# Optimization experiments

Hardware: AMD Instinct MI355X
Metric: run time of the kernel (lower is better)

The kernel has to match this reference:

```python
import jax, jax.numpy as jnp
import numpy as np

# Static config (matches init_kwargs)
B, S, D = 1, 2048, 2048
H, KVH, HD = 16, 4, 128
GROUPS = H // KVH
HEAVY_RATIO = 0.1
RECENT_RATIO = 0.1
SCALE = HD ** -0.5


def setup_inputs() -> dict:
    key = jax.random.key(0)
    ks = jax.random.split(key, 8)
    std = 0.02
    return {
        "hidden_states": jax.random.normal(ks[0], (B, S, D), jnp.float32),
        "q_w": jax.random.normal(ks[1], (D, H * HD), jnp.float32) * std,
        "q_b": jax.random.normal(ks[2], (H * HD,), jnp.float32) * std,
        "k_w": jax.random.normal(ks[3], (D, KVH * HD), jnp.float32) * std,
        "k_b": jax.random.normal(ks[4], (KVH * HD,), jnp.float32) * std,
        "v_w": jax.random.normal(ks[5], (D, KVH * HD), jnp.float32) * std,
        "v_b": jax.random.normal(ks[6], (KVH * HD,), jnp.float32) * std,
        "o_w": jax.random.normal(ks[7], (H * HD, D), jnp.float32) * std,
    }


def reference(hidden_states, q_w, q_b, k_w, k_b, v_w, v_b, o_w):
    # QKV projections -> [B, heads, S, HD]
    q = (hidden_states @ q_w + q_b).reshape(B, S, H, HD).transpose(0, 2, 1, 3)
    k = (hidden_states @ k_w + k_b).reshape(B, S, KVH, HD).transpose(0, 2, 1, 3)
    v = (hidden_states @ v_w + v_b).reshape(B, S, KVH, HD).transpose(0, 2, 1, 3)

    # GQA: repeat KV heads to match query heads (repeat_kv)
    k = jnp.repeat(k, GROUPS, axis=1)  # [B, H, S, HD]
    v = jnp.repeat(v, GROUPS, axis=1)

    # Scaled QK^T with additive causal mask (first call: no H2O mask yet)
    scores = jnp.einsum("bhqd,bhkd->bhqk", q, k) * SCALE
    causal = jnp.tril(jnp.ones((S, S), dtype=bool))
    scores = jnp.where(causal[None, None], scores, jnp.finfo(scores.dtype).min)

    # Softmax in fp32, cast back
    probs = jax.nn.softmax(scores.astype(jnp.float32), axis=-1).astype(q.dtype)

    # H2O heavy-hitter scoring: accumulate attn mass per key, per head
    cur_scores = probs.sum(axis=0).sum(axis=1)  # [H, S]

    heavy_budget = int(HEAVY_RATIO * S)
    recent_budget = int(RECENT_RATIO * S)

    # Eviction mask for next step: keep recent window + top-k heavy hitters
    attn_mask = jnp.ones((H, S + 1), dtype=probs.dtype)
    attn_mask = attn_mask.at[:, : S + 1 - recent_budget].set(0.0)
    selected = cur_scores[:, : S - recent_budget]  # scores outside recent window
    _, keep_topk = jax.lax.top_k(selected, heavy_budget)  # [H, heavy_budget]
    attn_mask = attn_mask.at[jnp.arange(H)[:, None], keep_topk].set(1.0)

    # Attention output + output projection
    out = jnp.einsum("bhqk,bhkd->bhqd", probs, v)
    out = out.transpose(0, 2, 1, 3).reshape(B, S, H * HD) @ o_w
    return out, attn_mask
```

## Files before the change

### kernel.cpp

```cpp
#include <hip/hip_runtime.h>
#include <hip/hip_bf16.h>
#include <math.h>

constexpr int S   = 2048;
constexpr int D   = 2048;
constexpr int H   = 16;
constexpr int KVH = 4;
constexpr int HD  = 128;
constexpr int NQ  = H * HD;
constexpr int NKV = KVH * HD;
constexpr int N3  = NQ + 2 * NKV;
constexpr int GROUPS = H / KVH;
constexpr float SCALE = 0.088388347648318447f;
constexpr int HEAVY  = 204;
constexpr int RECENT = 204;
constexpr int SKEEP  = S - RECENT;
constexpr int MASKC  = S + 1;
constexpr int NTILE_H = 528;

typedef short bf16x8 __attribute__((ext_vector_type(8)));
typedef _Float16 f16x8 __attribute__((ext_vector_type(8)));
typedef unsigned short ushort8 __attribute__((ext_vector_type(8)));
typedef unsigned short ushort4v __attribute__((ext_vector_type(4)));
typedef float f32x4 __attribute__((ext_vector_type(4)));

__device__ __forceinline__ unsigned short f2b(float x) {
  __hip_bfloat16 h = __float2bfloat16(x);
  return *(unsigned short*)&h;
}
__device__ __forceinline__ float b2f(unsigned short u) {
  __hip_bfloat16 h = *(__hip_bfloat16*)&u;
  return __bfloat162float(h);
}
__device__ __forceinline__ unsigned short f2h(float x) {
  _Float16 h = (_Float16)x;
  return *(unsigned short*)&h;
}

__device__ __forceinline__ void gload16(const unsigned short* g,
                                        unsigned short* l) {
  __builtin_amdgcn_global_load_lds(
      (const __attribute__((address_space(1))) unsigned int*)g,
      (__attribute__((address_space(3))) unsigned int*)l, 16, 0, 0);
}

__device__ __forceinline__ void split_wT_dev(
    const float* __restrict__ in, unsigned short* __restrict__ oh,
    unsigned short* __restrict__ ol, int K, int N, int rowOff, int ldOut,
    int bx, int by, float (*Lt)[65]) {
  const int n0 = bx * 64, k0 = by * 64;
  const int t = threadIdx.x;
  const int cq = t & 15, r4 = t >> 4;
#pragma unroll
  for (int i = 0; i < 4; ++i) {
    int r = r4 + i * 16;
    float4 v = *(const float4*)&in[(size_t)(k0 + r) * N + n0 + cq * 4];
    Lt[cq * 4 + 0][r] = v.x;
    Lt[cq * 4 + 1][r] = v.y;
    Lt[cq * 4 + 2][r] = v.z;
    Lt[cq * 4 + 3][r] = v.w;
  }
  __syncthreads();
#pragma unroll
  for (int i = 0; i < 4; ++i) {
    int rr = r4 + i * 16;
    size_t base = (size_t)(rowOff + n0 + rr) * ldOut + k0 + cq * 4;
    ushort4v hv, lv;
#pragma unroll
    for (int j = 0; j < 4; ++j) {
      float x = Lt[rr][cq * 4 + j];
      unsigned short h = f2b(x);
      hv[j] = h;
      lv[j] = f2b(x - b2f(h));
    }
    *(ushort4v*)&oh[base] = hv;
    *(ushort4v*)&ol[base] = lv;
  }
}

__global__ __launch_bounds__(256) void prep_all(
    const float* __restrict__ hs, const float* __restrict__ q_w,
    const float* __restrict__ k_w, const float* __restrict__ v_w,
    const float* __restrict__ o_w, const float* __restrict__ qb,
    const float* __restrict__ kb, const float* __restrict__ vb,
    unsigned short* __restrict__ hsh, unsigned short* __restrict__ hsl,
    unsigned short* __restrict__ WTh, unsigned short* __restrict__ WTl,
    unsigned short* __restrict__ OTh, float* __restrict__ bcat) {
  __shared__ float Lt[64][65];
  const int b = blockIdx.x;
  if (b < 1024) {
    split_wT_dev(q_w, WTh, WTl, D, NQ, 0, D, b & 31, b >> 5, Lt);
  } else if (b < 1280) {
    int b2 = b - 1024;
    split_wT_dev(k_w, WTh, WTl, D, NKV, NQ, D, b2 & 7, b2 >> 3, Lt);
  } else if (b < 1536) {
    int b2 = b - 1280;
    split_wT_dev(v_w, WTh, WTl, D, NKV, NQ + NKV, D, b2 & 7, b2 >> 3, Lt);
  } else if (b < 2560) {
    int b2 = b - 1536;
    const int n0 = (b2 & 31) * 64, k0 = (b2 >> 5) * 64;
    const int t = threadIdx.x;
    const int cq = t & 15, r4 = t >> 4;
#pragma unroll
    for (int i = 0; i < 4; ++i) {
      int r = r4 + i * 16;
      float4 v = *(const float4*)&o_w[(size_t)(k0 + r) * D + n0 + cq * 4];
      Lt[cq * 4 + 0][r] = v.x;
      Lt[cq * 4 + 1][r] = v.y;
      Lt[cq * 4 + 2][r] = v.z;
      Lt[cq * 4 + 3][r] = v.w;
    }
    __syncthreads();
#pragma unroll
    for (int i = 0; i < 4; ++i) {
      int rr = r4 + i * 16;
      size_t base = (size_t)(n0 + rr) * NQ + k0 + cq * 4;
      ushort4v hv;
#pragma unroll
      for (int j = 0; j < 4; ++j) hv[j] = f2b(Lt[rr][cq * 4 + j]);
      *(ushort4v*)&OTh[base] = hv;
    }
  } else if (b < 3072) {
    int b2 = b - 2560;
    size_t base = (size_t)b2 * 8192;
    for (int i = threadIdx.x * 4; i < 8192; i += 1024) {
      float4 v = *(const float4*)&hs[base + i];
      ushort4v hv, lv;
      float xs[4] = {v.x, v.y, v.z, v.w};
#pragma unroll
      for (int j = 0; j < 4; ++j) {
        unsigned short h = f2b(xs[j]);
        hv[j] = h;
        lv[j] = f2b(xs[j] - b2f(h));
      }
      *(ushort4v*)&hsh[base + i] = hv;
      *(ushort4v*)&hsl[base + i] = lv;
    }
  } else {
    int i = (b - 3072) * 256 + threadIdx.x;
    if (i < NQ) bcat[i] = qb[i];
    else if (i < NQ + NKV) bcat[i] = kb[i - NQ];
    else if (i < N3) bcat[i] = vb[i - NQ - NKV];
  }
}

__global__ __launch_bounds__(256) void gemm_qkv(
    const unsigned short* __restrict__ Ah, const unsigned short* __restrict__ Al,
    const unsigned short* __restrict__ Bh, const unsigned short* __restrict__ Bl,
    const float* __restrict__ bias,
    unsigned short* __restrict__ Qh,
    unsigned short* __restrict__ Kh,
    unsigned short* __restrict__ Vt, int M, int N, int K) {
  __shared__ __align__(16) unsigned short sAh[2][128 * 32];
  __shared__ __align__(16) unsigned short sAl[2][128 * 32];
  __shared__ __align__(16) unsigned short sBh[2][96 * 32];
  __shared__ __align__(16) unsigned short sBl[2][96 * 32];
  const int tid = threadIdx.x;
  const int lane = tid & 63, wave = tid >> 6;
  const int wm = wave >> 1, wn = wave & 1;
  const int quad = lane >> 4, l16 = lane & 15;
  const int m0 = blockIdx.y * 128, n0 = blockIdx.x * 96;

  const int lr = lane >> 2;
  const int gj = (lane & 3) ^ (lr & 3);

  f32x4 acc[4][3];
#pragma unroll
  for (int i = 0; i < 4; ++i)
#pragma unroll
    for (int j = 0; j < 3; ++j) acc[i][j] = (f32x4){0.f, 0.f, 0.f, 0.f};

#pragma unroll
  for (int it = 0; it < 2; ++it) {
    int c = wave * 2 + it;
    int r = c * 16 + lr;
    size_t ga = (size_t)(m0 + r) * K + gj * 8;
    gload16(&Ah[ga], &sAh[0][c * 512]);
    gload16(&Al[ga], &sAl[0][c * 512]);
  }
#pragma unroll
  for (int it = 0; it < 2; ++it) {
    int c = wave + it * 4;
    if (c < 6) {
      int r = c * 16 + lr;
      size_t gb = (size_t)(n0 + r) * K + gj * 8;
      gload16(&Bh[gb], &sBh[0][c * 512]);
      gload16(&Bl[gb], &sBl[0][c * 512]);
    }
  }
  __syncthreads();

  int cur = 0;
  for (int k0 = 0; k0 < K; k0 += 32, cur ^= 1) {
    if (k0 + 32 < K) {
      const int kn = k0 + 32;
#pragma unroll
      for (int it = 0; it < 2; ++it) {
        int c = wave * 2 + it;
        int r = c * 16 + lr;
        size_t ga = (size_t)(m0 + r) * K + kn + gj * 8;
        gload16(&Ah[ga], &sAh[cur ^ 1][c * 512]);
        gload16(&Al[ga], &sAl[cur ^ 1][c * 512]);
      }
#pragma unroll
      for (int it = 0; it < 2; ++it) {
        int c = wave + it * 4;
        if (c < 6) {
          int r = c * 16 + lr;
          size_t gb = (size_t)(n0 + r) * K + kn + gj * 8;
          gload16(&Bh[gb], &sBh[cur ^ 1][c * 512]);
          gload16(&Bl[gb], &sBl[cur ^ 1][c * 512]);
        }
      }
    }
    const int sw = (quad ^ (l16 & 3)) * 8;
    bf16x8 fah[4], fal[4], fbh[3], fbl[3];
#pragma unroll
    for (int i = 0; i < 4; ++i) {
      int ra = (wm * 64 + i * 16 + l16) * 32 + sw;
      fah[i] = *(bf16x8*)&sAh[cur][ra];
      fal[i] = *(bf16x8*)&sAl[cur][ra];
    }
#pragma unroll
    for (int j = 0; j < 3; ++j) {
      int rb = (wn * 48 + j * 16 + l16) * 32 + sw;
      fbh[j] = *(bf16x8*)&sBh[cur][rb];
      fbl[j] = *(bf16x8*)&sBl[cur][rb];
    }
#pragma unroll
    for (int i = 0; i < 4; ++i)
#pragma unroll
      for (int j = 0; j < 3; ++j) {
        acc[i][j] = __builtin_amdgcn_mfma_f32_16x16x32_bf16(fah[i], fbh[j], acc[i][j], 0, 0, 0);
        acc[i][j] = __builtin_amdgcn_mfma_f32_16x16x32_bf16(fah[i], fbl[j], acc[i][j], 0, 0, 0);
        acc[i][j] = __builtin_amdgcn_mfma_f32_16x16x32_bf16(fal[i], fbh[j], acc[i][j], 0, 0, 0);
      }
    __syncthreads();
  }
#pragma unroll
  for (int i = 0; i < 4; ++i) {
#pragma unroll
    for (int j = 0; j < 3; ++j) {
      int row = m0 + wm * 64 + i * 16 + quad * 4;
      int col = n0 + wn * 48 + j * 16 + l16;
      float bv = bias[col];
      if (col < NQ) {
#pragma unroll
        for (int r = 0; r < 4; ++r) {
          size_t o = (size_t)(row + r) * NQ + col;
          Qh[o] = f2h(acc[i][j][r] + bv);
        }
      } else if (col < NQ + NKV) {
        int c = col - NQ;
        size_t ob = ((size_t)(c >> 7) * S) * HD + (c & 127);
#pragma unroll
        for (int r = 0; r < 4; ++r) {
          size_t o = ob + (size_t)(row + r) * HD;
          Kh[o] = f2h(acc[i][j][r] + bv);
        }
      } else {
        int c = col - NQ - NKV;
        ushort4v pv;
#pragma unroll
        for (int r = 0; r < 4; ++r) pv[r] = f2h(acc[i][j][r] + bv);
        *(ushort4v*)&Vt[((size_t)(c >> 7) * HD + (c & 127)) * S + row] = pv;
      }
    }
  }
}

__global__ __launch_bounds__(256) void fuse_post(
    const unsigned short* __restrict__ AOh, const unsigned short* __restrict__ OTh,
    float* __restrict__ C,
    const unsigned short* __restrict__ Eg, const float* __restrict__ lbuf,
    float* __restrict__ cur) {
  __shared__ __align__(16) unsigned char smem[32768];
  const int bid = blockIdx.x;
  const int tid = threadIdx.x;
  if (bid < 256) {
    unsigned short* sAb = (unsigned short*)smem;
    unsigned short* sBb = (unsigned short*)smem + 8192;
    const int lane = tid & 63, wave = tid >> 6;
    const int wm = wave >> 1, wn = wave & 1;
    const int quad = lane >> 4, l16 = lane & 15;
    const int m0 = (bid >> 4) * 128, n0 = (bid & 15) * 128;
    const int K = NQ, N = D;
    const int lr = lane >> 2;
    const int gj = (lane & 3) ^ (lr & 3);

    f32x4 acc[4][4];
#pragma unroll
    for (int i = 0; i < 4; ++i)
#pragma unroll
      for (int j = 0; j < 4; ++j) acc[i][j] = (f32x4){0.f, 0.f, 0.f, 0.f};

#pragma unroll
    for (int it = 0; it < 2; ++it) {
      int c = wave * 2 + it;
      int r = c * 16 + lr;
      size_t ga = (size_t)(m0 + r) * K + gj * 8;
      size_t gb = (size_t)(n0 + r) * K + gj * 8;
      gload16(&AOh[ga], &sAb[c * 512]);
      gload16(&OTh[gb], &sBb[c * 512]);
    }
    __syncthreads();

    int cb = 0;
    for (int k0 = 0; k0 < K; k0 += 32, cb ^= 1) {
      if (k0 + 32 < K) {
        const int kn = k0 + 32;
#pragma unroll
        for (int it = 0; it < 2; ++it) {
          int c = wave * 2 + it;
          int r = c * 16 + lr;
          size_t ga = (size_t)(m0 + r) * K + kn + gj * 8;
          size_t gb = (size_t)(n0 + r) * K + kn + gj * 8;
          gload16(&AOh[ga], &sAb[(cb ^ 1) * 4096 + c * 512]);
          gload16(&OTh[gb], &sBb[(cb ^ 1) * 4096 + c * 512]);
        }
      }
      const int sw = (quad ^ (l16 & 3)) * 8;
      bf16x8 fa[4], fb[4];
#pragma unroll
      for (int i = 0; i < 4; ++i) {
        fa[i] = *(bf16x8*)&sAb[cb * 4096 + (wm * 64 + i * 16 + l16) * 32 + sw];
        fb[i] = *(bf16x8*)&sBb[cb * 4096 + (wn * 64 + i * 16 + l16) * 32 + sw];
      }
#pragma unroll
      for (int i = 0; i < 4; ++i)
#pragma unroll
        for (int j = 0; j < 4; ++j)
          acc[i][j] = __builtin_amdgcn_mfma_f32_16x16x32_bf16(fa[i], fb[j], acc[i][j], 0, 0, 0);
      __syncthreads();
    }
#pragma unroll
    for (int i = 0; i < 4; ++i)
#pragma unroll
      for (int j = 0; j < 4; ++j) {
        int row = m0 + wm * 64 + i * 16 + quad * 4;
        int col = n0 + wn * 64 + j * 16 + l16;
#pragma unroll
        for (int r = 0; r < 4; ++r)
          C[(size_t)(row + r) * N + col] = acc[i][j][r];
      }
  } else {
    const int bid2 = bid - 256;
    const int kt = bid2 % 29;
    const int h  = bid2 / 29;
    const int c8 = tid & 7, qg = tid >> 3;
    float acc[8];
#pragma unroll
    for (int j = 0; j < 8; ++j) acc[j] = 0.f;
    const size_t hb = (size_t)h * NTILE_H;
    for (int qt = kt; qt < 32; ++qt) {
      size_t tb = (hb + (size_t)(qt * (qt + 1) / 2) + kt) * 4096;
      float li0 = 1.0f / lbuf[h * S + qt * 64 + qg];
      float li1 = 1.0f / lbuf[h * S + qt * 64 + 32 + qg];
      f16x8 e0 = *(const f16x8*)&Eg[tb + (size_t)qg * 64 + c8 * 8];
      f16x8 e1 = *(const f16x8*)&Eg[tb + (size_t)(32 + qg) * 64 + c8 * 8];
#pragma unroll
      for (int j = 0; j < 8; ++j)
        acc[j] += (float)e0[j] * li0 + (float)e1[j] * li1;
    }
    float (*red)[8] = (float(*)[8])smem;
#pragma unroll
    for (int j = 0; j < 8; ++j) red[tid][j] = acc[j];
    __syncthreads();
    if (tid < 64) {
      int cc = tid >> 3, j = tid & 7;
      float s = 0.f;
#pragma unroll
      for (int g = 0; g < 32; ++g) s += red[cc + 8 * g][j];
      cur[h * S + kt * 64 + cc * 8 + j] = s;
    }
  }
}

__global__ __launch_bounds__(256) void gemm_bf16(
    const unsigned short* __restrict__ Ah, const unsigned short* __restrict__ Bh,
    float* __restrict__ C, int M, int N, int K) {
  __shared__ __align__(16) unsigned short sA[2][128 * 32];
  __shared__ __align__(16) unsigned short sB[2][128 * 32];
  const int tid = threadIdx.x;
  const int lane = tid & 63, wave = tid >> 6;
  const int wm = wave >> 1, wn = wave & 1;
  const int quad = lane >> 4, l16 = lane & 15;
  const int m0 = blockIdx.y * 128, n0 = blockIdx.x * 128;
  const int lr = lane >> 2;
  const int gj = (lane & 3) ^ (lr & 3);

  f32x4 acc[4][4];
#pragma unroll
  for (int i = 0; i < 4; ++i)
#pragma unroll
    for (int j = 0; j < 4; ++j) acc[i][j] = (f32x4){0.f, 0.f, 0.f, 0.f};

#pragma unroll
  for (int it = 0; it < 2; ++it) {
    int c = wave * 2 + it;
    int r = c * 16 + lr;
    size_t ga = (size_t)(m0 + r) * K + gj * 8;
    size_t gb = (size_t)(n0 + r) * K + gj * 8;
    gload16(&Ah[ga], &sA[0][c * 512]);
    gload16(&Bh[gb], &sB[0][c * 512]);
  }
  __syncthreads();

  int cur = 0;
  for (int k0 = 0; k0 < K; k0 += 32, cur ^= 1) {
    if (k0 + 32 < K) {
      const int kn = k0 + 32;
#pragma unroll
      for (int it = 0; it < 2; ++it) {
        int c = wave * 2 + it;
        int r = c * 16 + lr;
        size_t ga = (size_t)(m0 + r) * K + kn + gj * 8;
        size_t gb = (size_t)(n0 + r) * K + kn + gj * 8;
        gload16(&Ah[ga], &sA[cur ^ 1][c * 512]);
        gload16(&Bh[gb], &sB[cur ^ 1][c * 512]);
      }
    }
    const int sw = (quad ^ (l16 & 3)) * 8;
    bf16x8 fa[4], fb[4];
#pragma unroll
    for (int i = 0; i < 4; ++i) {
      fa[i] = *(bf16x8*)&sA[cur][(wm * 64 + i * 16 + l16) * 32 + sw];
      fb[i] = *(bf16x8*)&sB[cur][(wn * 64 + i * 16 + l16) * 32 + sw];
    }
#pragma unroll
    for (int i = 0; i < 4; ++i)
#pragma unroll
      for (int j = 0; j < 4; ++j)
        acc[i][j] = __builtin_amdgcn_mfma_f32_16x16x32_bf16(fa[i], fb[j], acc[i][j], 0, 0, 0);
    __syncthreads();
  }
#pragma unroll
  for (int i = 0; i < 4; ++i)
#pragma unroll
    for (int j = 0; j < 4; ++j) {
      int row = m0 + wm * 64 + i * 16 + quad * 4;
      int col = n0 + wn * 64 + j * 16 + l16;
#pragma unroll
      for (int r = 0; r < 4; ++r)
        C[(size_t)(row + r) * N + col] = acc[i][j][r];
    }
}

__global__ __launch_bounds__(256) void attn_mfma(
    const unsigned short* __restrict__ Qh,
    const unsigned short* __restrict__ Kh,
    const unsigned short* __restrict__ Vt, unsigned short* __restrict__ AOh,
    float* __restrict__ lbuf, unsigned short* __restrict__ Eg) {
  const int x = blockIdx.x;
  const int base = x & 255;
  const int qt0 = base & 31, h0 = base >> 5;
  const int qt = (x < 256) ? qt0 : 31 - qt0;
  const int h  = (x < 256) ? h0 : h0 + 8;
  const int kvh = h / GROUPS;
  const int tid = threadIdx.x;
  const int lane = tid & 63, w = tid >> 6;
  const int quad = lane >> 4, l16 = lane & 15;
  const int q0 = qt * 64;

  __shared__ __align__(16) unsigned short smem[22528];
  unsigned short* sQ  = smem;
  unsigned short* sK  = smem;
  unsigned short* sVt = smem + 8704;
  unsigned short* sP  = smem + 17920;

  const size_t ebase = ((size_t)h * NTILE_H + (size_t)(qt * (qt + 1) / 2)) * 4096;

  ushort8 pK[4], pV[4];
#pragma unroll
  for (int it = 0; it < 4; ++it) {
    int idx = tid + it * 256;
    int r = idx >> 4, c8 = idx & 15;
    size_t g = ((size_t)kvh * S + r) * HD + c8 * 8;
    pK[it] = *(const ushort8*)&Kh[g];
  }
#pragma unroll
  for (int it = 0; it < 4; ++it) {
    int idx = tid + it * 256;
    int d = idx >> 3, c8 = idx & 7;
    size_t g = ((size_t)kvh * HD + d) * S + c8 * 8;
    pV[it] = *(const ushort8*)&Vt[g];
  }

#pragma unroll
  for (int it = 0; it < 4; ++it) {
    int idx = tid + it * 256;
    int r = idx >> 4, c8 = idx & 15;
    size_t g = (size_t)(q0 + r) * NQ + h * HD + c8 * 8;
    *(ushort8*)&sQ[r * 136 + c8 * 8] = *(const ushort8*)&Qh[g];
  }
  __syncthreads();
  f16x8 fq[4];
#pragma unroll
  for (int d4 = 0; d4 < 4; ++d4)
    fq[d4] = *(f16x8*)&sQ[(w * 16 + l16) * 136 + d4 * 32 + quad * 8];

  f32x4 O[8];
#pragma unroll
  for (int jn = 0; jn < 8; ++jn) O[jn] = (f32x4){0.f, 0.f, 0.f, 0.f};
  float l_[4] = {0.f, 0.f, 0.f, 0.f};

  const int row_l = w * 16 + quad * 4;
  const int wbase = w * 1152;

  for (int kt = 0; kt <= qt; ++kt) {
    __syncthreads();
#pragma unroll
    for (int it = 0; it < 4; ++it) {
      int idx = tid + it * 256;
      int r = idx >> 4, c8 = idx & 15;
      *(ushort8*)&sK[r * 136 + c8 * 8] = pK[it];
    }
#pragma unroll
    for (int it = 0; it < 4; ++it) {
      int idx = tid + it * 256;
      int d = idx >> 3, c8 = idx & 7;
      *(ushort8*)&sVt[d * 72 + c8 * 8] = pV[it];
    }
    __syncthreads();
    if (kt < qt) {
#pragma unroll
      for (int it = 0; it < 4; ++it) {
        int idx = tid + it * 256;
        int r = idx >> 4, c8 = idx & 15;
        size_t g = ((size_t)kvh * S + (kt + 1) * 64 + r) * HD + c8 * 8;
        pK[it] = *(const ushort8*)&Kh[g];
      }
#pragma unroll
      for (int it = 0; it < 4; ++it) {
        int idx = tid + it * 256;
        int d = idx >> 3, c8 = idx & 7;
        size_t g = ((size_t)kvh * HD + d) * S + (kt + 1) * 64 + c8 * 8;
        pV[it] = *(const ushort8*)&Vt[g];
      }
    }

    f32x4 sc[4];
#pragma unroll
    for (int j = 0; j < 4; ++j) sc[j] = (f32x4){0.f, 0.f, 0.f, 0.f};
#pragma unroll
    for (int d4 = 0; d4 < 4; ++d4) {
#pragma unroll
      for (int j = 0; j < 4; ++j) {
        f16x8 bk = *(f16x8*)&sK[(j * 16 + l16) * 136 + d4 * 32 + quad * 8];
        sc[j] = __builtin_amdgcn_mfma_f32_16x16x32_f16(fq[d4], bk, sc[j], 0, 0, 0);
      }
    }
    const bool diag = (kt == qt);
#pragma unroll
    for (int j = 0; j < 4; ++j) {
      int col_l = j * 16 + l16;
#pragma unroll
      for (int r = 0; r < 4; ++r) {
        float v = sc[j][r] * SCALE;
        if (diag && col_l > row_l + r) v = -INFINITY;
        float p = __expf(v);
        sc[j][r] = p;
        l_[r] += p;
      }
    }
#pragma unroll
    for (int j = 0; j < 4; ++j)
#pragma unroll
      for (int r = 0; r < 4; ++r)
        sP[wbase + (quad * 4 + r) * 72 + j * 16 + l16] = f2h(sc[j][r]);

    if (Eg) {
      size_t tb = ebase + (size_t)kt * 4096;
#pragma unroll
      for (int it2 = 0; it2 < 2; ++it2) {
        int ci = lane + it2 * 64;
        int row = ci >> 3, cc = ci & 7;
        *(ushort8*)&Eg[tb + (size_t)(w * 16 + row) * 64 + cc * 8] =
            *(ushort8*)&sP[wbase + row * 72 + cc * 8];
      }
    }

    f16x8 ap0 = *(f16x8*)&sP[wbase + l16 * 72 + quad * 8];
    f16x8 ap1 = *(f16x8*)&sP[wbase + l16 * 72 + 32 + quad * 8];
#pragma unroll
    for (int jn = 0; jn < 8; ++jn) {
      f16x8 bv0 = *(f16x8*)&sVt[(jn * 16 + l16) * 72 + quad * 8];
      f16x8 bv1 = *(f16x8*)&sVt[(jn * 16 + l16) * 72 + 32 + quad * 8];
      O[jn] = __builtin_amdgcn_mfma_f32_16x16x32_f16(ap0, bv0, O[jn], 0, 0, 0);
      O[jn] = __builtin_amdgcn_mfma_f32_16x16x32_f16(ap1, bv1, O[jn], 0, 0, 0);
    }
  }
#pragma unroll
  for (int off = 1; off < 16; off <<= 1)
#pragma unroll
    for (int r = 0; r < 4; ++r) l_[r] += __shfl_xor(l_[r], off);
  float linv[4];
#pragma unroll
  for (int r = 0; r < 4; ++r) linv[r] = 1.0f / l_[r];
#pragma unroll
  for (int jn = 0; jn < 8; ++jn)
#pragma unroll
    for (int r = 0; r < 4; ++r)
      AOh[(size_t)(q0 + row_l + r) * NQ + h * HD + jn * 16 + l16] =
          f2b(O[jn][r] * linv[r]);
  if (l16 == 0) {
#pragma unroll
    for (int r = 0; r < 4; ++r)
      lbuf[h * S + q0 + row_l + r] = l_[r];
  }
}

__global__ __launch_bounds__(256) void cur_mfma(
    const unsigned short* __restrict__ Qh,
    const unsigned short* __restrict__ Kh,
    const float* __restrict__ lbuf, float* __restrict__ cur) {
  const int x = blockIdx.x;
  const int base = x & 255;
  const int kt0 = base & 31, h0 = base >> 5;
  const int kt = (x < 256) ? kt0 : 31 - kt0;
  const int h  = (x < 256) ? h0 : h0 + 8;
  const int kvh = h / GROUPS;
  const int tid = threadIdx.x;
  const int lane = tid & 63, w = tid >> 6;
  const int quad = lane >> 4, l16 = lane & 15;

  __shared__ __align__(16) unsigned short sKh[8704];
  __shared__ __align__(16) unsigned short sQh[8704];
  __shared__ float slinv[64];

#pragma unroll
  for (int it = 0; it < 4; ++it) {
    int idx = tid + it * 256;
    int r = idx >> 4, c8 = idx & 15;
    size_t g = ((size_t)kvh * S + kt * 64 + r) * HD + c8 * 8;
    *(ushort8*)&sKh[r * 136 + c8 * 8] = *(const ushort8*)&Kh[g];
  }
  __syncthreads();
  f16x8 fk[4];
#pragma unroll
  for (int d4 = 0; d4 < 4; ++d4)
    fk[d4] = *(f16x8*)&sKh[(w * 16 + l16) * 136 + d4 * 32 + quad * 8];

  const int krow_l = w * 16 + quad * 4;
  float csum[4] = {0.f, 0.f, 0.f, 0.f};

  ushort8 pQ[4];
  float pli = 0.f;
#pragma unroll
  for (int it = 0; it < 4; ++it) {
    int idx = tid + it * 256;
    int r = idx >> 4, c8 = idx & 15;
    size_t g = (size_t)(kt * 64 + r) * NQ + h * HD + c8 * 8;
    pQ[it] = *(const ushort8*)&Qh[g];
  }
  if (tid < 64) pli = 1.0f / lbuf[h * S + kt * 64 + tid];

  for (int qt = kt; qt < S / 64; ++qt) {
    __syncthreads();
#pragma unroll
    for (int it = 0; it < 4; ++it) {
      int idx = tid + it * 256;
      int r = idx >> 4, c8 = idx & 15;
      *(ushort8*)&sQh[r * 136 + c8 * 8] = pQ[it];
    }
    if (tid < 64) slinv[tid] = pli;
    __syncthreads();
    if (qt + 1 < S / 64) {
#pragma unroll
      for (int it = 0; it < 4; ++it) {
        int idx = tid + it * 256;
        int r = idx >> 4, c8 = idx & 15;
        size_t g = (size_t)((qt + 1) * 64 + r) * NQ + h * HD + c8 * 8;
        pQ[it] = *(const ushort8*)&Qh[g];
      }
      if (tid < 64) pli = 1.0f / lbuf[h * S + (qt + 1) * 64 + tid];
    }
    f32x4 sc[4];
#pragma unroll
    for (int j = 0; j < 4; ++j) sc[j] = (f32x4){0.f, 0.f, 0.f, 0.f};
#pragma unroll
    for (int d4 = 0; d4 < 4; ++d4) {
#pragma unroll
      for (int j = 0; j < 4; ++j) {
        f16x8 bq = *(f16x8*)&sQh[(j * 16 + l16) * 136 + d4 * 32 + quad * 8];
        sc[j] = __builtin_amdgcn_mfma_f32_16x16x32_f16(fk[d4], bq, sc[j], 0, 0, 0);
      }
    }
    const bool diag = (qt == kt);
#pragma unroll
    for (int j = 0; j < 4; ++j) {
      int qcol_l = j * 16 + l16;
      float lv = slinv[qcol_l];
#pragma unroll
      for (int r = 0; r < 4; ++r) {
        float p = __expf(sc[j][r] * SCALE) * lv;
        if (diag && (krow_l + r) > qcol_l) p = 0.f;
        csum[r] += p;
      }
    }
  }
#pragma unroll
  for (int off = 1; off < 16; off <<= 1)
#pragma unroll
    for (int r = 0; r < 4; ++r) csum[r] += __shfl_xor(csum[r], off);
  if (l16 == 0) {
#pragma unroll
    for (int r = 0; r < 4; ++r)
      cur[h * S + kt * 64 + krow_l + r] = csum[r];
  }
}

__global__ __launch_bounds__(256) void topk_kernel(
    const float* __restrict__ cur, float* __restrict__ mask) {
  const int h = blockIdx.x;
  const int tid = threadIdx.x;
  const int lane = tid & 63, w = tid >> 6;
  __shared__ unsigned uv[SKEEP];
  __shared__ int redw[4];
  __shared__ int wsum[4];

  for (int i = tid; i < SKEEP; i += 256) uv[i] = __float_as_uint(cur[h * S + i]);
  __syncthreads();

  unsigned lo = 0u, hi = 0xffffffffu;
  while (lo < hi) {
    unsigned mid = (unsigned)((((unsigned long long)lo + hi) + 1ull) >> 1);
    int c = 0;
    for (int i = tid; i < SKEEP; i += 256) c += (uv[i] >= mid) ? 1 : 0;
#pragma unroll
    for (int off = 1; off < 64; off <<= 1) c += __shfl_xor(c, off);
    if (lane == 0) redw[w] = c;
    __syncthreads();
    int cnt = redw[0] + redw[1] + redw[2] + redw[3];
    __syncthreads();
    if (cnt >= HEAVY) lo = mid; else hi = mid - 1;
  }
  const unsigned vk = lo;
  int c = 0;
  for (int i = tid; i < SKEEP; i += 256) c += (uv[i] > vk) ? 1 : 0;
#pragma unroll
  for (int off = 1; off < 64; off <<= 1) c += __shfl_xor(c, off);
  if (lane == 0) redw[w] = c;
  __syncthreads();
  const int cgt = redw[0] + redw[1] + redw[2] + redw[3];
  const int rem = HEAVY - cgt;

  for (int j = tid; j < MASKC; j += 256)
    mask[(size_t)h * MASKC + j] = (j >= MASKC - RECENT) ? 1.0f : 0.0f;
  __syncthreads();
  for (int i = tid; i < SKEEP; i += 256)
    if (uv[i] > vk) mask[(size_t)h * MASKC + i] = 1.0f;

  constexpr int PER = (SKEEP + 255) / 256;
  int i0 = tid * PER;
  int i1 = i0 + PER;
  if (i0 > SKEEP) i0 = SKEEP;
  if (i1 > SKEEP) i1 = SKEEP;
  int myT = 0;
  for (int i = i0; i < i1; ++i) myT += (uv[i] == vk) ? 1 : 0;
  int v = myT;
#pragma unroll
  for (int off = 1; off < 64; off <<= 1) {
    int t = __shfl_up(v, off);
    if (lane >= off) v += t;
  }
  if (lane == 63) wsum[w] = v;
  __syncthreads();
  int wOff = 0;
  for (int k = 0; k < w; ++k) wOff += wsum[k];
  int excl = wOff + v - myT;
  for (int i = i0; i < i1; ++i) {
    if (uv[i] == vk) {
      if (excl < rem) mask[(size_t)h * MASKC + i] = 1.0f;
      ++excl;
    }
  }
}

extern "C" void kernel_launch(void* const* d_in, const int* in_sizes, int n_in,
                              void* d_out, int out_size, void* d_ws,
                              size_t ws_size, hipStream_t stream) {
  const float* hs  = (const float*)d_in[0];
  const float* q_w = (const float*)d_in[1];
  const float* q_b = (const float*)d_in[2];
  const float* k_w = (const float*)d_in[3];
  const float* k_b = (const float*)d_in[4];
  const float* v_w = (const float*)d_in[5];
  const float* v_b = (const float*)d_in[6];
  const float* o_w = (const float*)d_in[7];

  char* ws = (char*)d_ws;
  unsigned short* Qh   = (unsigned short*)(ws + 0);
  unsigned short* Kh   = (unsigned short*)(ws + 16777216);
  unsigned short* Vt   = (unsigned short*)(ws + 20971520);
  unsigned short* AOh  = (unsigned short*)(ws + 25165824);
  float* lb   = (float*)(ws + 33685504);
  float* cur  = (float*)(ws + 33816576);
  float* bcat = (float*)(ws + 33947648);
  char* pool = ws + 33959936;
  unsigned short* hsh = (unsigned short*)pool;
  unsigned short* hsl = (unsigned short*)(pool + 8388608);
  unsigned short* WTh = (unsigned short*)(pool + 16777216);
  unsigned short* WTl = (unsigned short*)(pool + 29360128);
  unsigned short* OTh = (unsigned short*)(pool + 41943040);

  const size_t E_OFF = 84291584ull;
  const size_t E_SZ  = (size_t)H * NTILE_H * 4096 * 2;
  const bool use_e = (ws_size >= E_OFF + E_SZ);
  unsigned short* Eg = use_e ? (unsigned short*)(ws + E_OFF) : nullptr;

  float* outp  = (float*)d_out;
  float* maskp = outp + (size_t)S * D;

  dim3 blk(256);
  prep_all<<<dim3(3084), blk, 0, stream>>>(hs, q_w, k_w, v_w, o_w, q_b, k_b,
                                           v_b, hsh, hsl, WTh, WTl, OTh, bcat);
  gemm_qkv<<<dim3(N3 / 96, S / 128), blk, 0, stream>>>(
      hsh, hsl, WTh, WTl, bcat, Qh, Kh, Vt, S, N3, D);
  attn_mfma<<<dim3(512), blk, 0, stream>>>(Qh, Kh, Vt, AOh, lb, Eg);
  if (use_e) {
    fuse_post<<<dim3(256 + 29 * 16), blk, 0, stream>>>(AOh, OTh, outp, Eg, lb,
                                                       cur);
    topk_kernel<<<dim3(H), blk, 0, stream>>>(cur, maskp);
  } else {
    cur_mfma<<<dim3(512), blk, 0, stream>>>(Qh, Kh, lb, cur);
    topk_kernel<<<dim3(H), blk, 0, stream>>>(cur, maskp);
    gemm_bf16<<<dim3(D / 128, S / 128), blk, 0, stream>>>(AOh, OTh, outp, S, D,
                                                          NQ);
  }
}
```

Baseline: 289.5 us.

## Move o_w transpose into attention launch and halve output GEMM tile width

The o_w transpose/bf16 conversion moves out of prep_all and into 1024 extra blocks of the attn_mfma launch, where it can fill idle CUs alongside the causal-attention blocks. The output-projection part of fuse_post now uses 128x64 tiles (512 blocks instead of 256), giving more parallelism and a smaller shared-memory footprint. The tradeoff is more redundant A-tile loads across tiles. If use_e is false, the fallback gemm_bf16 still reads OTh, which is now produced by attn_mfma, so launch order still holds.

```diff
diff --git a/kernel.cpp b/kernel.cpp
--- a/kernel.cpp
+++ b/kernel.cpp
@@ -81,11 +81,11 @@
 __global__ __launch_bounds__(256) void prep_all(
     const float* __restrict__ hs, const float* __restrict__ q_w,
     const float* __restrict__ k_w, const float* __restrict__ v_w,
-    const float* __restrict__ o_w, const float* __restrict__ qb,
-    const float* __restrict__ kb, const float* __restrict__ vb,
+    const float* __restrict__ qb, const float* __restrict__ kb,
+    const float* __restrict__ vb,
     unsigned short* __restrict__ hsh, unsigned short* __restrict__ hsl,
     unsigned short* __restrict__ WTh, unsigned short* __restrict__ WTl,
-    unsigned short* __restrict__ OTh, float* __restrict__ bcat) {
+    float* __restrict__ bcat) {
   __shared__ float Lt[64][65];
   const int b = blockIdx.x;
   if (b < 1024) {
@@ -96,32 +96,8 @@
   } else if (b < 1536) {
     int b2 = b - 1280;
     split_wT_dev(v_w, WTh, WTl, D, NKV, NQ + NKV, D, b2 & 7, b2 >> 3, Lt);
-  } else if (b < 2560) {
+  } else if (b < 2048) {
     int b2 = b - 1536;
-    const int n0 = (b2 & 31) * 64, k0 = (b2 >> 5) * 64;
-    const int t = threadIdx.x;
-    const int cq = t & 15, r4 = t >> 4;
-#pragma unroll
-    for (int i = 0; i < 4; ++i) {
-      int r = r4 + i * 16;
-      float4 v = *(const float4*)&o_w[(size_t)(k0 + r) * D + n0 + cq * 4];
-      Lt[cq * 4 + 0][r] = v.x;
-      Lt[cq * 4 + 1][r] = v.y;
-      Lt[cq * 4 + 2][r] = v.z;
-      Lt[cq * 4 + 3][r] = v.w;
-    }
-    __syncthreads();
-#pragma unroll
-    for (int i = 0; i < 4; ++i) {
-      int rr = r4 + i * 16;
-      size_t base = (size_t)(n0 + rr) * NQ + k0 + cq * 4;
-      ushort4v hv;
-#pragma unroll
-      for (int j = 0; j < 4; ++j) hv[j] = f2b(Lt[rr][cq * 4 + j]);
-      *(ushort4v*)&OTh[base] = hv;
-    }
-  } else if (b < 3072) {
-    int b2 = b - 2560;
     size_t base = (size_t)b2 * 8192;
     for (int i = threadIdx.x * 4; i < 8192; i += 1024) {
       float4 v = *(const float4*)&hs[base + i];
@@ -137,7 +113,7 @@
       *(ushort4v*)&hsl[base + i] = lv;
     }
   } else {
-    int i = (b - 3072) * 256 + threadIdx.x;
+    int i = (b - 2048) * 256 + threadIdx.x;
     if (i < NQ) bcat[i] = qb[i];
     else if (i < NQ + NKV) bcat[i] = kb[i - NQ];
     else if (i < N3) bcat[i] = vb[i - NQ - NKV];
@@ -274,34 +250,37 @@
     float* __restrict__ C,
     const unsigned short* __restrict__ Eg, const float* __restrict__ lbuf,
     float* __restrict__ cur) {
-  __shared__ __align__(16) unsigned char smem[32768];
+  __shared__ __align__(16) unsigned char smem[24576];
   const int bid = blockIdx.x;
   const int tid = threadIdx.x;
-  if (bid < 256) {
+  if (bid < 512) {
     unsigned short* sAb = (unsigned short*)smem;
     unsigned short* sBb = (unsigned short*)smem + 8192;
     const int lane = tid & 63, wave = tid >> 6;
     const int wm = wave >> 1, wn = wave & 1;
     const int quad = lane >> 4, l16 = lane & 15;
-    const int m0 = (bid >> 4) * 128, n0 = (bid & 15) * 128;
+    const int m0 = (bid >> 5) * 128, n0 = (bid & 31) * 64;
     const int K = NQ, N = D;
     const int lr = lane >> 2;
     const int gj = (lane & 3) ^ (lr & 3);
 
-    f32x4 acc[4][4];
+    f32x4 acc[4][2];
 #pragma unroll
     for (int i = 0; i < 4; ++i)
 #pragma unroll
-      for (int j = 0; j < 4; ++j) acc[i][j] = (f32x4){0.f, 0.f, 0.f, 0.f};
+      for (int j = 0; j < 2; ++j) acc[i][j] = (f32x4){0.f, 0.f, 0.f, 0.f};
 
 #pragma unroll
     for (int it = 0; it < 2; ++it) {
       int c = wave * 2 + it;
       int r = c * 16 + lr;
       size_t ga = (size_t)(m0 + r) * K + gj * 8;
+      gload16(&AOh[ga], &sAb[c * 512]);
+    }
+    {
+      int r = wave * 16 + lr;
       size_t gb = (size_t)(n0 + r) * K + gj * 8;
-      gload16(&AOh[ga], &sAb[c * 512]);
-      gload16(&OTh[gb], &sBb[c * 512]);
+      gload16(&OTh[gb], &sBb[wave * 512]);
     }
     __syncthreads();
 
@@ -314,37 +293,41 @@
           int c = wave * 2 + it;
           int r = c * 16 + lr;
           size_t ga = (size_t)(m0 + r) * K + kn + gj * 8;
+          gload16(&AOh[ga], &sAb[(cb ^ 1) * 4096 + c * 512]);
+        }
+        {
+          int r = wave * 16 + lr;
           size_t gb = (size_t)(n0 + r) * K + kn + gj * 8;
-          gload16(&AOh[ga], &sAb[(cb ^ 1) * 4096 + c * 512]);
-          gload16(&OTh[gb], &sBb[(cb ^ 1) * 4096 + c * 512]);
+          gload16(&OTh[gb], &sBb[(cb ^ 1) * 2048 + wave * 512]);
         }
       }
       const int sw = (quad ^ (l16 & 3)) * 8;
-      bf16x8 fa[4], fb[4];
-#pragma unroll
-      for (int i = 0; i < 4; ++i) {
+      bf16x8 fa[4], fb[2];
+#pragma unroll
+      for (int i = 0; i < 4; ++i)
         fa[i] = *(bf16x8*)&sAb[cb * 4096 + (wm * 64 + i * 16 + l16) * 32 + sw];
-        fb[i] = *(bf16x8*)&sBb[cb * 4096 + (wn * 64 + i * 16 + l16) * 32 + sw];
-      }
+#pragma unroll
+      for (int j = 0; j < 2; ++j)
+        fb[j] = *(bf16x8*)&sBb[cb * 2048 + (wn * 32 + j * 16 + l16) * 32 + sw];
 #pragma unroll
       for (int i = 0; i < 4; ++i)
 #pragma unroll
-        for (int j = 0; j < 4; ++j)
+        for (int j = 0; j < 2; ++j)
           acc[i][j] = __builtin_amdgcn_mfma_f32_16x16x32_bf16(fa[i], fb[j], acc[i][j], 0, 0, 0);
       __syncthreads();
     }
 #pragma unroll
     for (int i = 0; i < 4; ++i)
 #pragma unroll
-      for (int j = 0; j < 4; ++j) {
+      for (int j = 0; j < 2; ++j) {
         int row = m0 + wm * 64 + i * 16 + quad * 4;
-        int col = n0 + wn * 64 + j * 16 + l16;
+        int col = n0 + wn * 32 + j * 16 + l16;
 #pragma unroll
         for (int r = 0; r < 4; ++r)
           C[(size_t)(row + r) * N + col] = acc[i][j][r];
       }
   } else {
-    const int bid2 = bid - 256;
+    const int bid2 = bid - 512;
     const int kt = bid2 % 29;
     const int h  = bid2 / 29;
     const int c8 = tid & 7, qg = tid >> 3;
@@ -450,19 +433,49 @@
     const unsigned short* __restrict__ Qh,
     const unsigned short* __restrict__ Kh,
     const unsigned short* __restrict__ Vt, unsigned short* __restrict__ AOh,
-    float* __restrict__ lbuf, unsigned short* __restrict__ Eg) {
+    float* __restrict__ lbuf, unsigned short* __restrict__ Eg,
+    const float* __restrict__ o_w, unsigned short* __restrict__ OTh) {
   const int x = blockIdx.x;
+  const int tid = threadIdx.x;
+
+  __shared__ __align__(16) unsigned short smem[22528];
+
+  if (x >= 512) {
+    float (*Lt)[65] = (float(*)[65])smem;
+    int b2 = x - 512;
+    const int n0 = (b2 & 31) * 64, k0 = (b2 >> 5) * 64;
+    const int cq = tid & 15, r4 = tid >> 4;
+#pragma unroll
+    for (int i = 0; i < 4; ++i) {
+      int r = r4 + i * 16;
+      float4 v = *(const float4*)&o_w[(size_t)(k0 + r) * D + n0 + cq * 4];
+      Lt[cq * 4 + 0][r] = v.x;
+      Lt[cq * 4 + 1][r] = v.y;
+      Lt[cq * 4 + 2][r] = v.z;
+      Lt[cq * 4 + 3][r] = v.w;
+    }
+    __syncthreads();
+#pragma unroll
+    for (int i = 0; i < 4; ++i) {
+      int rr = r4 + i * 16;
+      size_t base = (size_t)(n0 + rr) * NQ + k0 + cq * 4;
+      ushort4v hv;
+#pragma unroll
+      for (int j = 0; j < 4; ++j) hv[j] = f2b(Lt[rr][cq * 4 + j]);
+      *(ushort4v*)&OTh[base] = hv;
+    }
+    return;
+  }
+
   const int base = x & 255;
   const int qt0 = base & 31, h0 = base >> 5;
   const int qt = (x < 256) ? qt0 : 31 - qt0;
   const int h  = (x < 256) ? h0 : h0 + 8;
   const int kvh = h / GROUPS;
-  const int tid = threadIdx.x;
   const int lane = tid & 63, w = tid >> 6;
   const int quad = lane >> 4, l16 = lane & 15;
   const int q0 = qt * 64;
 
-  __shared__ __align__(16) unsigned short smem[22528];
   unsigned short* sQ  = smem;
   unsigned short* sK  = smem;
   unsigned short* sVt = smem + 8704;
@@ -813,13 +826,13 @@
   float* maskp = outp + (size_t)S * D;
 
   dim3 blk(256);
-  prep_all<<<dim3(3084), blk, 0, stream>>>(hs, q_w, k_w, v_w, o_w, q_b, k_b,
-                                           v_b, hsh, hsl, WTh, WTl, OTh, bcat);
+  prep_all<<<dim3(2060), blk, 0, stream>>>(hs, q_w, k_w, v_w, q_b, k_b, v_b,
+                                           hsh, hsl, WTh, WTl, bcat);
   gemm_qkv<<<dim3(N3 / 96, S / 128), blk, 0, stream>>>(
       hsh, hsl, WTh, WTl, bcat, Qh, Kh, Vt, S, N3, D);
-  attn_mfma<<<dim3(512), blk, 0, stream>>>(Qh, Kh, Vt, AOh, lb, Eg);
+  attn_mfma<<<dim3(1536), blk, 0, stream>>>(Qh, Kh, Vt, AOh, lb, Eg, o_w, OTh);
   if (use_e) {
-    fuse_post<<<dim3(256 + 29 * 16), blk, 0, stream>>>(AOh, OTh, outp, Eg, lb,
+    fuse_post<<<dim3(512 + 29 * 16), blk, 0, stream>>>(AOh, OTh, outp, Eg, lb,
                                                        cur);
     topk_kernel<<<dim3(H), blk, 0, stream>>>(cur, maskp);
   } else {
```

New measurement: 293.5 us. No clear change (+1.4%).

## Split KV range for long query tiles in attention and add combine kernel

Applied to the files above, without the earlier changes.

For query tiles in the upper half of the causal triangle, the attention kernel now splits the key range into two halves handled by separate blocks. Each block writes unnormalized fp32 partial outputs and row sums, and a new combine kernel adds them, normalizes, and writes the bf16 output and row sums. The aim is to shorten the critical path of the longest causal tiles and improve load balance, raising the grid from 512 to 768 blocks. The cost is an extra kernel launch and fp32 partial-result traffic, and the path only runs when the workspace is large enough.

```diff
diff --git a/kernel.cpp b/kernel.cpp
--- a/kernel.cpp
+++ b/kernel.cpp
@@ -450,17 +450,43 @@
     const unsigned short* __restrict__ Qh,
     const unsigned short* __restrict__ Kh,
     const unsigned short* __restrict__ Vt, unsigned short* __restrict__ AOh,
-    float* __restrict__ lbuf, unsigned short* __restrict__ Eg) {
+    float* __restrict__ lbuf, unsigned short* __restrict__ Eg,
+    int do_split, float* __restrict__ Opart, float* __restrict__ lpart) {
   const int x = blockIdx.x;
-  const int base = x & 255;
-  const int qt0 = base & 31, h0 = base >> 5;
-  const int qt = (x < 256) ? qt0 : 31 - qt0;
-  const int h  = (x < 256) ? h0 : h0 + 8;
-  const int kvh = h / GROUPS;
   const int tid = threadIdx.x;
   const int lane = tid & 63, w = tid >> 6;
   const int quad = lane >> 4, l16 = lane & 15;
+
+  int qt, h, kt0, kt1, part = 0;
+  bool partial = false;
+  if (do_split) {
+    if (x < 512) {
+      qt = 31 - (x >> 5);
+      int r5 = x & 31;
+      h = r5 >> 1;
+      part = r5 & 1;
+      int nh = (qt + 1) >> 1;
+      kt0 = part ? nh : 0;
+      kt1 = part ? qt + 1 : nh;
+      partial = true;
+    } else {
+      int s2 = x - 512;
+      qt = 15 - (s2 >> 4);
+      h = s2 & 15;
+      kt0 = 0;
+      kt1 = qt + 1;
+    }
+  } else {
+    const int base = x & 255;
+    const int qt0v = base & 31, h0 = base >> 5;
+    qt = (x < 256) ? qt0v : 31 - qt0v;
+    h  = (x < 256) ? h0 : h0 + 8;
+    kt0 = 0;
+    kt1 = qt + 1;
+  }
+  const int kvh = h / GROUPS;
   const int q0 = qt * 64;
+  const int pairIdx = partial ? ((qt - 16) * 16 + h) : 0;
 
   __shared__ __align__(16) unsigned short smem[22528];
   unsigned short* sQ  = smem;
@@ -475,14 +501,14 @@
   for (int it = 0; it < 4; ++it) {
     int idx = tid + it * 256;
     int r = idx >> 4, c8 = idx & 15;
-    size_t g = ((size_t)kvh * S + r) * HD + c8 * 8;
+    size_t g = ((size_t)kvh * S + kt0 * 64 + r) * HD + c8 * 8;
     pK[it] = *(const ushort8*)&Kh[g];
   }
 #pragma unroll
   for (int it = 0; it < 4; ++it) {
     int idx = tid + it * 256;
     int d = idx >> 3, c8 = idx & 7;
-    size_t g = ((size_t)kvh * HD + d) * S + c8 * 8;
+    size_t g = ((size_t)kvh * HD + d) * S + kt0 * 64 + c8 * 8;
     pV[it] = *(const ushort8*)&Vt[g];
   }
 
@@ -507,7 +533,7 @@
   const int row_l = w * 16 + quad * 4;
   const int wbase = w * 1152;
 
-  for (int kt = 0; kt <= qt; ++kt) {
+  for (int kt = kt0; kt < kt1; ++kt) {
     __syncthreads();
 #pragma unroll
     for (int it = 0; it < 4; ++it) {
@@ -522,7 +548,7 @@
       *(ushort8*)&sVt[d * 72 + c8 * 8] = pV[it];
     }
     __syncthreads();
-    if (kt < qt) {
+    if (kt + 1 < kt1) {
 #pragma unroll
       for (int it = 0; it < 4; ++it) {
         int idx = tid + it * 256;
@@ -594,19 +620,62 @@
   for (int off = 1; off < 16; off <<= 1)
 #pragma unroll
     for (int r = 0; r < 4; ++r) l_[r] += __shfl_xor(l_[r], off);
-  float linv[4];
-#pragma unroll
-  for (int r = 0; r < 4; ++r) linv[r] = 1.0f / l_[r];
-#pragma unroll
-  for (int jn = 0; jn < 8; ++jn)
-#pragma unroll
-    for (int r = 0; r < 4; ++r)
-      AOh[(size_t)(q0 + row_l + r) * NQ + h * HD + jn * 16 + l16] =
-          f2b(O[jn][r] * linv[r]);
-  if (l16 == 0) {
-#pragma unroll
-    for (int r = 0; r < 4; ++r)
-      lbuf[h * S + q0 + row_l + r] = l_[r];
+
+  if (partial) {
+    float* Ob = Opart + (size_t)(pairIdx * 2 + part) * 8192;
+#pragma unroll
+    for (int jn = 0; jn < 8; ++jn)
+#pragma unroll
+      for (int r = 0; r < 4; ++r)
+        Ob[(row_l + r) * 128 + jn * 16 + l16] = O[jn][r];
+    if (l16 == 0) {
+#pragma unroll
+      for (int r = 0; r < 4; ++r)
+        lpart[(pairIdx * 2 + part) * 64 + row_l + r] = l_[r];
+    }
+  } else {
+    float linv[4];
+#pragma unroll
+    for (int r = 0; r < 4; ++r) linv[r] = 1.0f / l_[r];
+#pragma unroll
+    for (int jn = 0; jn < 8; ++jn)
+#pragma unroll
+      for (int r = 0; r < 4; ++r)
+        AOh[(size_t)(q0 + row_l + r) * NQ + h * HD + jn * 16 + l16] =
+            f2b(O[jn][r] * linv[r]);
+    if (l16 == 0) {
+#pragma unroll
+      for (int r = 0; r < 4; ++r)
+        lbuf[h * S + q0 + row_l + r] = l_[r];
+    }
+  }
+}
+
+__global__ __launch_bounds__(256) void combine_o(
+    const float* __restrict__ Opart, const float* __restrict__ lpart,
+    unsigned short* __restrict__ AOh, float* __restrict__ lbuf) {
+  const int p = blockIdx.x;
+  const int qt = 16 + (p >> 4), h = p & 15;
+  const int q0 = qt * 64;
+  const int tid = threadIdx.x;
+  const int row = tid >> 2, cg = tid & 3;
+  const float l0 = lpart[(p * 2) * 64 + row];
+  const float l1 = lpart[(p * 2 + 1) * 64 + row];
+  const float lsum = l0 + l1;
+  const float linv = 1.0f / lsum;
+  if (cg == 0) lbuf[h * S + q0 + row] = lsum;
+  const float* O0 = Opart + ((size_t)(p * 2) * 64 + row) * 128 + cg * 32;
+  const float* O1 = Opart + ((size_t)(p * 2 + 1) * 64 + row) * 128 + cg * 32;
+  unsigned short* dst = AOh + (size_t)(q0 + row) * NQ + h * HD + cg * 32;
+  for (int c = 0; c < 32; c += 4) {
+    float4 a = *(const float4*)&O0[c];
+    float4 b = *(const float4*)&O1[c];
+    ushort4v o;
+    o[0] = f2b((a.x + b.x) * linv);
+    o[1] = f2b((a.y + b.y) * linv);
+    o[2] = f2b((a.z + b.z) * linv);
+    o[3] = f2b((a.w + b.w) * linv);
+    *(ushort4v*)&dst[c] = o;
   }
 }
 
@@ -809,6 +878,13 @@
   const bool use_e = (ws_size >= E_OFF + E_SZ);
   unsigned short* Eg = use_e ? (unsigned short*)(ws + E_OFF) : nullptr;
 
+  const size_t OPART_OFF = 153497600ull;
+  const size_t LPART_OFF = 170274816ull;
+  const size_t SPLIT_END = 170405888ull;
+  const bool use_split = use_e && (ws_size >= SPLIT_END);
+  float* Opart = (float*)(ws + OPART_OFF);
+  float* lpart = (float*)(ws + LPART_OFF);
+
   float* outp  = (float*)d_out;
   float* maskp = outp + (size_t)S * D;
 
@@ -817,7 +893,10 @@
                                            v_b, hsh, hsl, WTh, WTl, OTh, bcat);
   gemm_qkv<<<dim3(N3 / 96, S / 128), blk, 0, stream>>>(
       hsh, hsl, WTh, WTl, bcat, Qh, Kh, Vt, S, N3, D);
-  attn_mfma<<<dim3(512), blk, 0, stream>>>(Qh, Kh, Vt, AOh, lb, Eg);
+  attn_mfma<<<dim3(use_split ? 768 : 512), blk, 0, stream>>>(
+      Qh, Kh, Vt, AOh, lb, Eg, use_split ? 1 : 0, Opart, lpart);
+  if (use_split)
+    combine_o<<<dim3(256), blk, 0, stream>>>(Opart, lpart, AOh, lb);
   if (use_e) {
     fuse_post<<<dim3(256 + 29 * 16), blk, 0, stream>>>(AOh, OTh, outp, Eg, lb,
                                                        cur);
```

Measured after the change: 310.9 us. 1.07x slower.
